# Kernel tuning notes

Measured on AMD Instinct MI355X. Metric: run time of the kernel, lower is better.

## Reference

```python
import jax, jax.numpy as jnp
import numpy as np

CONF_TH = 0.6      # confidence_threshold
IOU_TH = 0.45      # iou_threshold
MAX_WH = 4096.0    # class offset for class-aware NMS (agnostic=False)
TOP_K = 1024       # fixed candidate cap (analog of max_nms, jit-static)
MAX_DET = 300      # max detections per image
NC = 80
AGNOSTIC = False


def setup_inputs() -> dict:
    key = jax.random.key(0)
    k1, k2 = jax.random.split(key)
    prediction = jax.random.uniform(k1, (16, 25200, 85), dtype=jnp.float32)
    logits = jax.random.uniform(k2, (16, 25200, 80), dtype=jnp.float32)
    return {"prediction": prediction, "logits": logits}


def xywh2xyxy(b):
    cx, cy, w, h = b[:, 0], b[:, 1], b[:, 2], b[:, 3]
    return jnp.stack([cx - w * 0.5, cy - h * 0.5, cx + w * 0.5, cy + h * 0.5], axis=-1)


def box_iou(a, b):
    # a: [K,4], b: [K,4] in xyxy -> [K,K] IoU
    area_a = (a[:, 2] - a[:, 0]) * (a[:, 3] - a[:, 1])
    area_b = (b[:, 2] - b[:, 0]) * (b[:, 3] - b[:, 1])
    lt = jnp.maximum(a[:, None, :2], b[None, :, :2])
    rb = jnp.minimum(a[:, None, 2:], b[None, :, 2:])
    wh = jnp.clip(rb - lt, 0.0)
    inter = wh[..., 0] * wh[..., 1]
    return inter / (area_a[:, None] + area_b[None, :] - inter + 1e-9)


def _greedy_keep(iou, valid):
    # iou: [K,K] on score-descending boxes; valid: [K] bool
    K = iou.shape[0]
    ar = jnp.arange(K)

    def step(suppressed, i):
        keep_i = valid[i] & ~suppressed[i]
        suppressed = suppressed | (keep_i & (iou[i] > IOU_TH) & (ar > i))
        return suppressed, keep_i

    _, keep = jax.lax.scan(step, jnp.zeros((K,), dtype=bool), ar)
    return keep


def _nms_image(pred, logit):
    # pred: [N, 5+nc], logit: [N, nc]
    obj = pred[:, 4]
    cls_scores = pred[:, 5:] * obj[:, None]          # x[:,5:] *= x[:,4:5]
    conf = jnp.max(cls_scores, axis=-1)              # best-class confidence
    cls = jnp.argmax(cls_scores, axis=-1)
    valid = (obj > CONF_TH) & (conf > CONF_TH)       # xc gate + conf gate
    box = xywh2xyxy(pred[:, :4])

    score = jnp.where(valid, conf, -1.0)
    top_scores, idx = jax.lax.top_k(score, TOP_K)    # descending-score candidates
    box_k = box[idx]                                  # [K,4] original boxes
    cls_k = cls[idx]
    logit_k = logit[idx]
    valid_k = top_scores > CONF_TH

    # class-aware offset (agnostic=False) for NMS only
    off = 0.0 if AGNOSTIC else MAX_WH
    nms_boxes = box_k + cls_k[:, None].astype(box_k.dtype) * off

    iou = box_iou(nms_boxes, nms_boxes)
    keep = _greedy_keep(iou, valid_k)

    kept_score = jnp.where(keep, top_scores, -1.0)
    sel_score, sel = jax.lax.top_k(kept_score, MAX_DET)
    out_valid = sel_score > CONF_TH

    det = jnp.concatenate(
        [box_k[sel], top_scores[sel][:, None], cls_k[sel][:, None].astype(jnp.float32)],
        axis=1,
    )  # [max_det, 6] = [xyxy, conf, cls]
    det = jnp.where(out_valid[:, None], det, 0.0)
    logits_out = jnp.where(out_valid[:, None], logit_k[sel], 0.0)  # [max_det, nc]
    return det, out_valid, logits_out


def reference(prediction, logits):
    det, valid, logits_out = jax.vmap(_nms_image)(prediction, logits)
    return det, valid, logits_out
```

## Files before the change

kernel.cpp:

```cpp
#include <hip/hip_runtime.h>
#include <stdint.h>

#define CONF_THR 0.6f
#define IOU_THR  0.45f
#define MAX_WH_F 4096.0f
#define TOPK     1024
#define MAX_DET  300
#define NCLS     80
#define ROW      85
#define APB      128
#define NMS_P    32

typedef unsigned int u32;
typedef unsigned long long u64;

__device__ __forceinline__ u32 f2s(float f) {
    u32 b = __float_as_uint(f);
    return b ^ ((u32)((int)b >> 31) | 0x80000000u);
}
__device__ __forceinline__ float s2f(u32 k) {
    u32 b = (k & 0x80000000u) ? (k ^ 0x80000000u) : ~k;
    return __uint_as_float(b);
}

__global__ __launch_bounds__(256) void k_score(const float* __restrict__ pred,
        u32* __restrict__ key, u32* __restrict__ cls, int NA) {
#pragma clang fp contract(off)
    int img = blockIdx.y;
    int a0 = blockIdx.x * APB;
    int count = min(APB, NA - a0);
    if (count <= 0) return;
    size_t baseoff = ((size_t)img * NA + a0) * ROW;
    const float* base = pred + baseoff;
    __shared__ __align__(16) float tile[APB * ROW];
    int nfloat = count * ROW;
    if ((baseoff & 3) == 0) {
        int nvec = nfloat >> 2;
        const float4* b4 = (const float4*)base;
        float4* t4 = (float4*)tile;
        for (int i = threadIdx.x; i < nvec; i += blockDim.x) t4[i] = b4[i];
        for (int i = (nvec << 2) + threadIdx.x; i < nfloat; i += blockDim.x)
            tile[i] = base[i];
    } else {
        for (int i = threadIdx.x; i < nfloat; i += blockDim.x) tile[i] = base[i];
    }
    __syncthreads();
    int t = threadIdx.x;
    if (t < count) {
        const float* r = tile + t * ROW;
        float obj = r[4];
        float maxv = -1.0f; int cl = 0;
        for (int j = 0; j < NCLS; ++j) {
            float v = r[5 + j] * obj;
            if (v > maxv) { maxv = v; cl = j; }
        }
        bool valid = (obj > CONF_THR) && (maxv > CONF_THR);
        float score = valid ? maxv : -1.0f;
        size_t g = (size_t)img * NA + a0 + t;
        key[g] = f2s(score);
        cls[g] = (u32)cl;
    }
}

__global__ __launch_bounds__(1024) void k_topk(const u32* __restrict__ key,
        u32* __restrict__ top_idx, float* __restrict__ top_score, int NA) {
    int img = blockIdx.x;
    const u32* kb = key + (size_t)img * NA;
    __shared__ u32 hist[256];
    __shared__ u32 sfx[256];
    __shared__ int sh_d;
    __shared__ u32 sh_t;
    __shared__ u32 gcnt, tie_base;
    __shared__ u32 wave_tot[16];
    __shared__ u64 skey[TOPK];
    int tid = threadIdx.x;
    u32 prefix = 0, target = TOPK;
    for (int level = 0; level < 4; ++level) {
        int shift = 24 - 8 * level;
        if (tid < 256) hist[tid] = 0;
        __syncthreads();
        for (int idx = tid; idx < NA; idx += 1024) {
            u32 k = kb[idx];
            bool in = (level == 0) || ((k >> (shift + 8)) == prefix);
            if (in) atomicAdd(&hist[(k >> shift) & 0xFFu], 1u);
        }
        __syncthreads();
        if (tid < 256) sfx[tid] = hist[tid];
        __syncthreads();
        for (int off = 1; off < 256; off <<= 1) {
            u32 v = 0;
            if (tid < 256) {
                v = sfx[tid];
                if (tid + off < 256) v += sfx[tid + off];
            }
            __syncthreads();
            if (tid < 256) sfx[tid] = v;
            __syncthreads();
        }
        if (tid < 256) {
            u32 S = sfx[tid];
            u32 Snext = (tid == 255) ? 0u : sfx[tid + 1];
            if (S >= target && Snext < target) { sh_d = tid; sh_t = target - Snext; }
        }
        __syncthreads();
        prefix = (prefix << 8) | (u32)sh_d;
        target = sh_t;
        __syncthreads();
    }
    u32 cutv = prefix;
    u32 R = target;
    if (tid == 0) { gcnt = 0; tie_base = 0; }
    __syncthreads();
    int wid = tid >> 6, lane = tid & 63;
    u64 lanemask = (1ull << lane) - 1ull;
    for (int c0 = 0; c0 < NA; c0 += 1024) {
        int idx = c0 + tid;
        bool inb = idx < NA;
        u32 k = inb ? kb[idx] : 0u;
        bool isg = inb && (k > cutv);
        bool ist = inb && (k == cutv);
        if (isg) {
            u32 p = atomicAdd(&gcnt, 1u);
            skey[p] = ((u64)k << 32) | (u64)(u32)(NA - 1 - idx);
        }
        u64 ball = __ballot(ist);
        if (lane == 0) wave_tot[wid] = (u32)__popcll(ball);
        __syncthreads();
        u32 wbase = 0;
        for (int w = 0; w < wid; ++w) wbase += wave_tot[w];
        u32 rank = tie_base + wbase + (u32)__popcll(ball & lanemask);
        if (ist && rank < R)
            skey[(TOPK - R) + rank] = ((u64)k << 32) | (u64)(u32)(NA - 1 - idx);
        __syncthreads();
        if (tid == 0) {
            u32 tot = 0;
            for (int w = 0; w < 16; ++w) tot += wave_tot[w];
            tie_base += tot;
        }
        __syncthreads();
    }
    for (int k2 = 2; k2 <= TOPK; k2 <<= 1) {
        for (int j = k2 >> 1; j > 0; j >>= 1) {
            int i = tid, ixj = i ^ j;
            if (ixj > i) {
                u64 a = skey[i], b = skey[ixj];
                bool desc = ((i & k2) == 0);
                if ((a < b) == desc) { skey[i] = b; skey[ixj] = a; }
            }
            __syncthreads();
        }
    }
    u64 kk = skey[tid];
    u32 aidx = (u32)(NA - 1) - (u32)(kk & 0xFFFFFFFFull);
    top_idx[img * TOPK + tid] = aidx;
    top_score[img * TOPK + tid] = s2f((u32)(kk >> 32));
}

__global__ void k_prep(const float* __restrict__ pred, const u32* __restrict__ cls,
        const u32* __restrict__ top_idx,
        float* __restrict__ boxk, float* __restrict__ nmsbox,
        float* __restrict__ clsf, int NA) {
#pragma clang fp contract(off)
    int img = blockIdx.y;
    int t = blockIdx.x * blockDim.x + threadIdx.x;
    if (t >= TOPK) return;
    int g = img * TOPK + t;
    u32 aidx = top_idx[g];
    const float* r = pred + ((size_t)img * NA + aidx) * ROW;
    float cx = r[0], cy = r[1], w = r[2], h = r[3];
    float hw = w * 0.5f, hh = h * 0.5f;
    float x1 = cx - hw, y1 = cy - hh, x2 = cx + hw, y2 = cy + hh;
    u32 c = cls[(size_t)img * NA + aidx];
    float off = (float)c * MAX_WH_F;
    boxk[g * 4 + 0] = x1; boxk[g * 4 + 1] = y1;
    boxk[g * 4 + 2] = x2; boxk[g * 4 + 3] = y2;
    nmsbox[g * 4 + 0] = x1 + off; nmsbox[g * 4 + 1] = y1 + off;
    nmsbox[g * 4 + 2] = x2 + off; nmsbox[g * 4 + 3] = y2 + off;
    clsf[g] = (float)c;
}

__global__ __launch_bounds__(1024) void k_mask(const float* __restrict__ nmsbox,
        u64* __restrict__ mask) {
#pragma clang fp contract(off)
    int img = blockIdx.y;
    __shared__ float bx[TOPK + 32], by[TOPK + 32], bX[TOPK + 32], bY[TOPK + 32], ar[TOPK + 32];
    int tid = threadIdx.x;
    {
        const float4* nb = (const float4*)(nmsbox + (size_t)img * TOPK * 4);
        float4 b = nb[tid];
        int pi = tid + (tid >> 5);
        bx[pi] = b.x; by[pi] = b.y; bX[pi] = b.z; bY[pi] = b.w;
        ar[pi] = (b.z - b.x) * (b.w - b.y);
    }
    __syncthreads();
    int i = blockIdx.x * 64 + (tid >> 4);
    int w = tid & 15;
    int pi = i + (i >> 5);
    float ax = bx[pi], ay = by[pi], aX = bX[pi], aY = bY[pi], aa = ar[pi];
    u64 bits = 0;
    for (int jj = 0; jj < 64; ++jj) {
        int j = (w << 6) + jj;
        if (j > i) {
            int pj = j + (j >> 5);
            float ltx = fmaxf(ax, bx[pj]);
            float lty = fmaxf(ay, by[pj]);
            float rbx = fminf(aX, bX[pj]);
            float rby = fminf(aY, bY[pj]);
            float ww = fmaxf(rbx - ltx, 0.0f);
            float hh = fmaxf(rby - lty, 0.0f);
            float inter = ww * hh;
            float denom = ((aa + ar[pj]) - inter) + 1e-9f;
            float iou = inter / denom;
            if (iou > IOU_THR) bits |= (1ull << jj);
        }
    }
    mask[((size_t)img * TOPK + i) * 16 + w] = bits;
}

__global__ __launch_bounds__(64) void k_nms(const u64* __restrict__ mask,
        const float* __restrict__ top_score,
        u32* __restrict__ sel, u32* __restrict__ selcnt) {
    int img = blockIdx.x;
    int lane = threadIdx.x;
    const u64* mrow = mask + (size_t)img * TOPK * 16;
    int cnt = 0;
    for (int k = 0; k < TOPK / 64; ++k) {
        float s = top_score[img * TOPK + k * 64 + lane];
        cnt += (s > CONF_THR) ? 1 : 0;
    }
    for (int off = 32; off > 0; off >>= 1) cnt += __shfl_down(cnt, off);
    int nvalid = __shfl(cnt, 0);

    bool ld = lane < 16;
    u64 rem = 0;
    u64 buf[NMS_P];
#pragma unroll
    for (int k = 0; k < NMS_P; ++k)
        buf[k] = (ld && k < TOPK) ? mrow[(size_t)k * 16 + lane] : 0ull;
    int kept = 0;
    for (int base = 0; base < TOPK; base += NMS_P) {
        if (base >= nvalid || kept >= MAX_DET) break;
#pragma unroll
        for (int k = 0; k < NMS_P; ++k) {
            int i = base + k;
            u64 roww = buf[k];
            int pf = i + NMS_P;
            buf[k] = (ld && pf < TOPK) ? mrow[(size_t)pf * 16 + lane] : 0ull;
            if (i < nvalid && kept < MAX_DET) {
                int w = i >> 6, b = i & 63;
                u64 rw = __shfl(rem, w);
                if (!((rw >> b) & 1ull)) {
                    if (lane == 0) sel[img * MAX_DET + kept] = (u32)i;
                    rem |= roww;
                    ++kept;
                }
            }
        }
    }
    if (lane == 0) selcnt[img] = (u32)kept;
}

__global__ void k_out(const float* __restrict__ logits,
        const u32* __restrict__ top_idx, const float* __restrict__ top_score,
        const float* __restrict__ boxk, const float* __restrict__ clsf,
        const u32* __restrict__ sel, const u32* __restrict__ selcnt,
        float* __restrict__ out, int NA, int B) {
    int img = blockIdx.y;
    int t = blockIdx.x;
    int tid = threadIdx.x;
    u32 K = selcnt[img];
    size_t detoff = ((size_t)img * MAX_DET + t) * 6;
    size_t voff = (size_t)B * MAX_DET * 6 + (size_t)img * MAX_DET + t;
    size_t loff = (size_t)B * MAX_DET * 7 + ((size_t)img * MAX_DET + t) * NCLS;
    if ((u32)t < K) {
        int slot = (int)sel[img * MAX_DET + t];
        int g = img * TOPK + slot;
        u32 aidx = top_idx[g];
        if (tid < NCLS)      out[loff + tid] = logits[((size_t)img * NA + aidx) * NCLS + tid];
        else if (tid < 84)   out[detoff + (tid - 80)] = boxk[(size_t)g * 4 + (tid - 80)];
        else if (tid == 84)  out[detoff + 4] = top_score[g];
        else if (tid == 85)  out[detoff + 5] = clsf[g];
        else if (tid == 86)  out[voff] = 1.0f;
    } else {
        if (tid < NCLS)      out[loff + tid] = 0.0f;
        else if (tid < 86)   out[detoff + (tid - 80)] = 0.0f;
        else if (tid == 86)  out[voff] = 0.0f;
    }
}

extern "C" void kernel_launch(void* const* d_in, const int* in_sizes, int n_in,
                              void* d_out, int out_size, void* d_ws, size_t ws_size,
                              hipStream_t stream) {
    const float* pred = (const float*)d_in[0];
    const float* logits = (const float*)d_in[1];
    float* out = (float*)d_out;
    const int B = out_size / (MAX_DET * (6 + 1 + NCLS));
    const int NA = in_sizes[0] / (B * ROW);

    char* p = (char*)d_ws;
    auto alloc = [&](size_t bytes) -> void* {
        void* r = (void*)p;
        p += (bytes + 255) & ~(size_t)255;
        return r;
    };
    u32* key       = (u32*)alloc((size_t)B * NA * 4);
    u32* cls       = (u32*)alloc((size_t)B * NA * 4);
    u32* top_idx   = (u32*)alloc((size_t)B * TOPK * 4);
    float* top_scr = (float*)alloc((size_t)B * TOPK * 4);
    float* boxk    = (float*)alloc((size_t)B * TOPK * 16);
    float* nmsbox  = (float*)alloc((size_t)B * TOPK * 16);
    float* clsf    = (float*)alloc((size_t)B * TOPK * 4);
    u64* mask      = (u64*)alloc((size_t)B * TOPK * 16 * 8);
    u32* sel       = (u32*)alloc((size_t)B * MAX_DET * 4);
    u32* selcnt    = (u32*)alloc((size_t)B * 4);

    k_score<<<dim3((NA + APB - 1) / APB, B), 256, 0, stream>>>(pred, key, cls, NA);
    k_topk<<<dim3(B), 1024, 0, stream>>>(key, top_idx, top_scr, NA);
    k_prep<<<dim3(TOPK / 256, B), 256, 0, stream>>>(pred, cls, top_idx, boxk, nmsbox, clsf, NA);
    k_mask<<<dim3(TOPK / 64, B), 1024, 0, stream>>>(nmsbox, mask);
    k_nms<<<dim3(B), 64, 0, stream>>>(mask, top_scr, sel, selcnt);
    k_out<<<dim3(MAX_DET, B), 128, 0, stream>>>(logits, top_idx, top_scr, boxk, clsf,
                                                sel, selcnt, out, NA, B);
}
```

Before: 448.4 us.

## Aggregate histogram atomics per wave and drop per-chunk barriers in top-k compaction

In the radix-select histogram, lanes of a wave that share the same digit are grouped with eight ballots, and only a leader lane does the shared-memory atomic add. The compaction pass now reserves slots with one atomic per wave and no longer calls __syncthreads per chunk. Ties at the cutoff key are resolved in a separate single-wave ordered scan, which runs only when not every tied element can be taken. The NMS loop also replaces a shuffle of the suppression word with a ballot. Together these cut atomic contention and barrier counts, at the cost of extra ballot instructions per histogram element.

```diff
diff --git a/kernel.cpp b/kernel.cpp
--- a/kernel.cpp
+++ b/kernel.cpp
@@ -70,19 +70,32 @@
     __shared__ u32 sfx[256];
     __shared__ int sh_d;
     __shared__ u32 sh_t;
-    __shared__ u32 gcnt, tie_base;
-    __shared__ u32 wave_tot[16];
+    __shared__ u32 gcnt;
     __shared__ u64 skey[TOPK];
     int tid = threadIdx.x;
+    int lane = tid & 63;
+    u64 lanemask = (1ull << lane) - 1ull;
     u32 prefix = 0, target = TOPK;
     for (int level = 0; level < 4; ++level) {
         int shift = 24 - 8 * level;
         if (tid < 256) hist[tid] = 0;
         __syncthreads();
-        for (int idx = tid; idx < NA; idx += 1024) {
-            u32 k = kb[idx];
-            bool in = (level == 0) || ((k >> (shift + 8)) == prefix);
-            if (in) atomicAdd(&hist[(k >> shift) & 0xFFu], 1u);
+        for (int idx0 = 0; idx0 < NA; idx0 += 1024) {
+            int idx = idx0 + tid;
+            bool inb = idx < NA;
+            u32 k = inb ? kb[idx] : 0u;
+            bool in = inb && ((level == 0) || ((k >> (shift + 8)) == prefix));
+            u32 d = (k >> shift) & 0xFFu;
+            u64 peers = __ballot(in);
+#pragma unroll
+            for (int bit = 0; bit < 8; ++bit) {
+                u64 bb = __ballot((d >> bit) & 1u);
+                peers &= ((d >> bit) & 1u) ? bb : ~bb;
+            }
+            if (in) {
+                int leader = (int)(__ffsll((long long)peers) - 1);
+                if (lane == leader) atomicAdd(&hist[d], (u32)__popcll(peers));
+            }
         }
         __syncthreads();
         if (tid < 256) sfx[tid] = hist[tid];
@@ -109,33 +122,41 @@
     }
     u32 cutv = prefix;
     u32 R = target;
-    if (tid == 0) { gcnt = 0; tie_base = 0; }
+    u32 T = hist[cutv & 0xFFu];
+    if (tid == 0) gcnt = 0;
     __syncthreads();
-    int wid = tid >> 6, lane = tid & 63;
-    u64 lanemask = (1ull << lane) - 1ull;
+    bool takeTies = (T == R);
     for (int c0 = 0; c0 < NA; c0 += 1024) {
         int idx = c0 + tid;
         bool inb = idx < NA;
         u32 k = inb ? kb[idx] : 0u;
-        bool isg = inb && (k > cutv);
-        bool ist = inb && (k == cutv);
-        if (isg) {
-            u32 p = atomicAdd(&gcnt, 1u);
-            skey[p] = ((u64)k << 32) | (u64)(u32)(NA - 1 - idx);
-        }
-        u64 ball = __ballot(ist);
-        if (lane == 0) wave_tot[wid] = (u32)__popcll(ball);
-        __syncthreads();
-        u32 wbase = 0;
-        for (int w = 0; w < wid; ++w) wbase += wave_tot[w];
-        u32 rank = tie_base + wbase + (u32)__popcll(ball & lanemask);
-        if (ist && rank < R)
-            skey[(TOPK - R) + rank] = ((u64)k << 32) | (u64)(u32)(NA - 1 - idx);
-        __syncthreads();
-        if (tid == 0) {
-            u32 tot = 0;
-            for (int w = 0; w < 16; ++w) tot += wave_tot[w];
-            tie_base += tot;
+        bool put = inb && ((k > cutv) || (takeTies && k == cutv));
+        u64 ball = __ballot(put);
+        if (ball) {
+            int leader = (int)(__ffsll((long long)ball) - 1);
+            u32 base = 0;
+            if (lane == leader) base = atomicAdd(&gcnt, (u32)__popcll(ball));
+            base = __shfl(base, leader);
+            if (put)
+                skey[base + (u32)__popcll(ball & lanemask)] =
+                    ((u64)k << 32) | (u64)(u32)(NA - 1 - idx);
+        }
+    }
+    __syncthreads();
+    if (!takeTies) {
+        u32 G = gcnt;
+        if (tid < 64) {
+            u32 cnt = 0;
+            for (int c0 = 0; c0 < NA; c0 += 64) {
+                int idx = c0 + tid;
+                bool ist = (idx < NA) && (kb[idx] == cutv);
+                u64 ball = __ballot(ist);
+                u32 rank = cnt + (u32)__popcll(ball & lanemask);
+                if (ist && rank < R)
+                    skey[G + rank] = ((u64)cutv << 32) | (u64)(u32)(NA - 1 - idx);
+                cnt += (u32)__popcll(ball);
+                if (cnt >= R) break;
+            }
         }
         __syncthreads();
     }
@@ -236,7 +257,7 @@
     u64 buf[NMS_P];
 #pragma unroll
     for (int k = 0; k < NMS_P; ++k)
-        buf[k] = (ld && k < TOPK) ? mrow[(size_t)k * 16 + lane] : 0ull;
+        buf[k] = ld ? mrow[(size_t)k * 16 + lane] : 0ull;
     int kept = 0;
     for (int base = 0; base < TOPK; base += NMS_P) {
         if (base >= nvalid || kept >= MAX_DET) break;
@@ -247,9 +268,8 @@
             int pf = i + NMS_P;
             buf[k] = (ld && pf < TOPK) ? mrow[(size_t)pf * 16 + lane] : 0ull;
             if (i < nvalid && kept < MAX_DET) {
-                int w = i >> 6, b = i & 63;
-                u64 rw = __shfl(rem, w);
-                if (!((rw >> b) & 1ull)) {
+                bool notsup = (lane == (i >> 6)) && !((rem >> (i & 63)) & 1ull);
+                if (__ballot(notsup) != 0ull) {
                     if (lane == 0) sel[img * MAX_DET + kept] = (u32)i;
                     rem |= roww;
                     ++kept;
```

Measured after the change: 454.8 us. Within noise of the previous version (+1.4%).
